# Kernel optimization log

Measured on AMD Instinct MI355X. Metric: run time of the kernel, lower is better.

Reference implementation:

```python
import jax, jax.numpy as jnp
import numpy as np

DIVERSITY_RATE = 0.5


def setup_inputs() -> dict:
    key = jax.random.key(0)
    k1, k2 = jax.random.split(key)
    # model log-probabilities at current step: (bsz, beam, vocab)
    lprobs = jax.nn.log_softmax(
        jax.random.normal(k1, (128, 5, 50257), dtype=jnp.float32), axis=-1
    )
    # historical hypothesis scores: (bsz, beam, step)
    scores = jax.random.normal(k2, (128, 5, 10), dtype=jnp.float32)
    return {"lprobs": lprobs, "scores": scores, "step": 10}


def reference(lprobs, scores, step):
    bsz, beam_size, vocab_size = lprobs.shape
    k = min(beam_size * 2, beam_size * vocab_size - 1)  # = 10 here

    # step > 0 path: accumulate running score of each hypothesis
    lp = lprobs + scores[:, :, step - 1][:, :, None]  # (bsz, beam, vocab)

    # 1/ per-beam top-k over vocab (vectorized over all beams at once)
    s, idx = jax.lax.top_k(lp, k)  # (bsz, beam, k); idx already < vocab (fmod no-op)

    # 2/,3/ intra-sibling ordering -> rank penalty (rank r gets r*rate)
    sibling_score = jnp.arange(1, k + 1, dtype=lp.dtype) * DIVERSITY_RATE  # (k,)
    s = s - sibling_score  # broadcast over (bsz, beam, k)

    # 4/ final top-k over all beam*k candidates
    indices = idx.reshape(bsz, beam_size * k)
    final_scores, flat_pos = jax.lax.top_k(s.reshape(bsz, beam_size * k), k)
    final_beams = flat_pos // k  # which input beam each winner came from
    final_indices = jnp.take_along_axis(indices, flat_pos, axis=1)  # vocab ids

    return final_scores, final_indices, final_beams
```

## Files before the change

### kernel.cpp

```cpp
#include <hip/hip_runtime.h>
#include <hip/hip_bf16.h>
#include <math.h>
#include <stdint.h>


#define BS   256
#define KK   10
#define BEAM 5
#define CAP  2048

typedef unsigned long long u64;

__device__ __forceinline__ uint32_t ford(float x) {
    uint32_t u = __float_as_uint(x);
    return (u & 0x80000000u) ? ~u : (u | 0x80000000u);
}
__device__ __forceinline__ float funord(uint32_t u) {
    return __uint_as_float((u & 0x80000000u) ? (u & 0x7fffffffu) : ~u);
}

__device__ __forceinline__ void merge_tree(u64* skey, int tid) {
    for (int off = BS / 2; off >= 1; off >>= 1) {
        if (tid < off) {
            const int pa = tid * KK, pb = (tid + off) * KK;
            u64 mk[KK];
            int ia = 0, ib = 0;
#pragma unroll
            for (int j = 0; j < KK; ++j) {
                u64 ka = skey[pa + ia], kb = skey[pb + ib];
                bool takeA = (ka >= kb);
                mk[j] = takeA ? ka : kb;
                if (takeA) ++ia; else ++ib;
            }
#pragma unroll
            for (int j = 0; j < KK; ++j) skey[pa + j] = mk[j];
        }
        __syncthreads();
    }
}

__global__ __launch_bounds__(BS) void dss_stage1(
    const float* __restrict__ lprobs,
    const float* __restrict__ scores,
    const int*   __restrict__ step_ptr,
    int vocab, int sdim,
    float* __restrict__ ws_val,
    int*   __restrict__ ws_idx)
{
    const int row = blockIdx.x;
    const int tid = threadIdx.x;
    const int step = step_ptr[0];
    const float bias = scores[(size_t)row * sdim + (step - 1)];
    const float* rp = lprobs + (size_t)row * vocab;

    __shared__ u64  cand[CAP];
    __shared__ u64  skey[BS * KK];
    __shared__ int  cnt;
    __shared__ float s_tau;

    int pre = (4 - (int)(((uintptr_t)rp >> 2) & 3)) & 3;
    if (pre > vocab) pre = vocab;
    const float4* p4 = (const float4*)(rp + pre);
    const int nvec = (vocab - pre) >> 2;
    const int done = pre + 4 * nvec;
    const int rem  = vocab - done;

    float m = -INFINITY;
    if (tid < pre) m = rp[tid];
#pragma unroll 4
    for (int t = tid; t < nvec; t += BS) {
        float4 x = p4[t];
        m = fmaxf(m, fmaxf(fmaxf(x.x, x.y), fmaxf(x.z, x.w)));
    }
    if (tid < rem) m = fmaxf(m, rp[done + tid]);

    {
        u64 key[KK];
        key[0] = ((u64)ford(m) << 32) | (uint32_t)~tid;
#pragma unroll
        for (int j = 1; j < KK; ++j) key[j] = 0;
#pragma unroll
        for (int j = 0; j < KK; ++j) skey[tid * KK + j] = key[j];
    }
    if (tid == 0) cnt = 0;
    __syncthreads();
    merge_tree(skey, tid);
    if (tid == 0) s_tau = funord((uint32_t)(skey[9] >> 32));
    __syncthreads();
    const float tau = s_tau;

    auto app = [&](float x, int i) {
        if (x >= tau) {
            int p = atomicAdd(&cnt, 1);
            if (p < CAP) cand[p] = ((u64)ford(x) << 32) | (uint32_t)~i;
        }
    };
    if (tid < pre) app(rp[tid], tid);
#pragma unroll 4
    for (int t = tid; t < nvec; t += BS) {
        float4 x = p4[t];
        int base = pre + 4 * t;
        if (x.x >= tau) app(x.x, base + 0);
        if (x.y >= tau) app(x.y, base + 1);
        if (x.z >= tau) app(x.z, base + 2);
        if (x.w >= tau) app(x.w, base + 3);
    }
    if (tid < rem) app(rp[done + tid], done + tid);
    __syncthreads();

    const int n = (cnt < CAP) ? cnt : CAP;
    {
        u64 key[KK];
#pragma unroll
        for (int j = 0; j < KK; ++j) key[j] = 0;
        for (int i = tid; i < n; i += BS) {
            u64 k = cand[i];
            if (k > key[KK - 1]) {
#pragma unroll
                for (int j = KK - 1; j >= 1; --j)
                    key[j] = (k > key[j - 1]) ? key[j - 1] : ((k > key[j]) ? k : key[j]);
                if (k > key[0]) key[0] = k;
            }
        }
#pragma unroll
        for (int j = 0; j < KK; ++j) skey[tid * KK + j] = key[j];
    }
    __syncthreads();
    merge_tree(skey, tid);

    if (tid < KK) {
        u64 k = skey[tid];
        ws_val[row * KK + tid] = funord((uint32_t)(k >> 32)) + bias;
        ws_idx[row * KK + tid] = (int)~(uint32_t)k;
    }
}

__global__ __launch_bounds__(64) void dss_stage2(
    const float* __restrict__ ws_val,
    const int*   __restrict__ ws_idx,
    float* __restrict__ out, int bsz)
{
    const int b = blockIdx.x;
    const int lane = threadIdx.x;

    float v = -INFINITY;
    int   vidx = 0;
    if (lane < BEAM * KK) {
        int beam = lane / KK;
        int r    = lane % KK;
        int o    = (b * BEAM + beam) * KK + r;
        v    = ws_val[o] - 0.5f * (float)(r + 1);
        vidx = ws_idx[o];
    }

    float* out_scores  = out;
    float* out_indices = out + (size_t)bsz * KK;
    float* out_beams   = out + 2 * (size_t)bsz * KK;

    for (int o = 0; o < KK; ++o) {
        float rv = v; int rp = lane;
#pragma unroll
        for (int off = 32; off >= 1; off >>= 1) {
            float ov = __shfl_xor(rv, off);
            int   op = __shfl_xor(rp, off);
            if (ov > rv || (ov == rv && op < rp)) { rv = ov; rp = op; }
        }
        int widx = __shfl(vidx, rp);
        if (lane == 0) {
            out_scores [b * KK + o] = rv;
            out_indices[b * KK + o] = (float)widx;
            out_beams  [b * KK + o] = (float)(rp / KK);
        }
        if (lane == rp) v = -INFINITY;
    }
}

extern "C" void kernel_launch(void* const* d_in, const int* in_sizes, int n_in,
                              void* d_out, int out_size, void* d_ws, size_t ws_size,
                              hipStream_t stream)
{
    const float* lprobs = (const float*)d_in[0];
    const float* scores = (const float*)d_in[1];
    const int*   step   = (const int*)d_in[2];

    const int bsz   = 128;
    const int rows  = bsz * BEAM;
    const int vocab = in_sizes[0] / rows;
    const int sdim  = in_sizes[1] / rows;

    float* ws_val = (float*)d_ws;
    int*   ws_idx = (int*)((char*)d_ws + (size_t)rows * KK * sizeof(float));

    dss_stage1<<<rows, BS, 0, stream>>>(lprobs, scores, step, vocab, sdim, ws_val, ws_idx);
    dss_stage2<<<bsz, 64, 0, stream>>>(ws_val, ws_idx, (float*)d_out, bsz);
}
```

Baseline: 225.8 us.

## Split each vocab row into chunks across blocks with LDS-staged two-pass top-k

Each row's vocab is split into up to 8 chunks, each handled by its own block, which gives 5120 blocks instead of 640 to fill the GPU. Every chunk block stages its slice in LDS so the second threshold pass reads shared memory rather than global memory. It picks the threshold with a wave-level shuffle top-10 in place of the tree merge. A new final kernel merges the per-chunk top-10 lists per beam and then runs the cross-beam selection. This trades extra workspace traffic and dynamic LDS use for more parallelism and a single global read of the input.

Measured after the change: 252.0 us. 1.12x slower.

```diff
diff --git a/kernel.cpp b/kernel.cpp
--- a/kernel.cpp
+++ b/kernel.cpp
@@ -7,7 +7,8 @@
 #define BS   256
 #define KK   10
 #define BEAM 5
-#define CAP  2048
+#define CAP  512
+#define FCAP 2048
 
 typedef unsigned long long u64;
 
@@ -19,33 +20,138 @@
     return __uint_as_float((u & 0x80000000u) ? (u & 0x7fffffffu) : ~u);
 }
 
-__device__ __forceinline__ void merge_tree(u64* skey, int tid) {
-    for (int off = BS / 2; off >= 1; off >>= 1) {
-        if (tid < off) {
-            const int pa = tid * KK, pb = (tid + off) * KK;
-            u64 mk[KK];
-            int ia = 0, ib = 0;
-#pragma unroll
-            for (int j = 0; j < KK; ++j) {
-                u64 ka = skey[pa + ia], kb = skey[pb + ib];
-                bool takeA = (ka >= kb);
-                mk[j] = takeA ? ka : kb;
-                if (takeA) ++ia; else ++ib;
-            }
-#pragma unroll
-            for (int j = 0; j < KK; ++j) skey[pa + j] = mk[j];
-        }
-        __syncthreads();
-    }
-}
-
-__global__ __launch_bounds__(BS) void dss_stage1(
+__device__ __forceinline__ void insert10(u64 (&key)[KK], u64 k) {
+    if (k > key[KK - 1]) {
+#pragma unroll
+        for (int j = KK - 1; j >= 1; --j)
+            key[j] = (k > key[j - 1]) ? key[j - 1] : ((k > key[j]) ? k : key[j]);
+        if (k > key[0]) key[0] = k;
+    }
+}
+
+extern __shared__ __align__(16) unsigned char smem_raw[];
+
+__global__ __launch_bounds__(BS) void dss_chunk_topk(
+    const float* __restrict__ lprobs,
+    const float* __restrict__ scores,
+    const int*   __restrict__ step_ptr,
+    int vocab, int sdim, int nc, int cs, int cap_f,
+    u64* __restrict__ ws_keys)
+{
+    const int chunk = blockIdx.x;
+    const int row   = blockIdx.y;
+    const int tid   = threadIdx.x;
+    const int lane  = tid & 63;
+    const int step  = step_ptr[0];
+    const float bias = scores[(size_t)row * sdim + (step - 1)];
+
+    const int c0 = chunk * cs;
+    int len = vocab - c0; if (len > cs) len = cs;
+    const float* rp = lprobs + (size_t)row * vocab + c0;
+
+    float* lds_f = (float*)smem_raw;
+    u64*   cand  = (u64*)(smem_raw + (size_t)cap_f * 4);
+    float* smax  = (float*)(cand + CAP);
+    int*   s_cnt = (int*)(smax + BS);
+    float* s_tau = (float*)(s_cnt + 1);
+
+    const int a0  = (int)(((uintptr_t)rp >> 2) & 3);
+    int pre = (4 - a0) & 3; if (pre > len) pre = len;
+    const float4* g4  = (const float4*)(rp + pre);
+    const int nvec = (len - pre) >> 2;
+    const int done = pre + 4 * nvec;
+    const int rem  = len - done;
+    float4* l4 = (float4*)(lds_f + a0 + pre);
+
+    float m = -INFINITY;
+    if (tid < pre) { float v = rp[tid] + bias; lds_f[a0 + tid] = v; m = v; }
+    for (int t = tid; t < nvec; t += BS) {
+        float4 x = g4[t];
+        x.x += bias; x.y += bias; x.z += bias; x.w += bias;
+        l4[t] = x;
+        m = fmaxf(m, fmaxf(fmaxf(x.x, x.y), fmaxf(x.z, x.w)));
+    }
+    if (tid < rem) { float v = rp[done + tid] + bias; lds_f[a0 + done + tid] = v; m = fmaxf(m, v); }
+
+    smax[tid] = m;
+    if (tid == 0) *s_cnt = 0;
+    __syncthreads();
+
+    if (tid < 64) {
+        float a = smax[lane], b = smax[lane + 64], c = smax[lane + 128], d = smax[lane + 192];
+        float t0;
+        if (a < b) { t0 = a; a = b; b = t0; }
+        if (c < d) { t0 = c; c = d; d = t0; }
+        if (a < c) { t0 = a; a = c; c = t0; }
+        if (b < d) { t0 = b; b = d; d = t0; }
+        if (b < c) { t0 = b; b = c; c = t0; }
+        float arr0 = a, arr1 = b, arr2 = c, arr3 = d;
+        float tau = -INFINITY;
+#pragma unroll
+        for (int r = 0; r < KK; ++r) {
+            float rv = arr0; int rl = lane;
+#pragma unroll
+            for (int o = 32; o >= 1; o >>= 1) {
+                float ov = __shfl_xor(rv, o);
+                int   ol = __shfl_xor(rl, o);
+                if (ov > rv || (ov == rv && ol < rl)) { rv = ov; rl = ol; }
+            }
+            if (lane == rl) { arr0 = arr1; arr1 = arr2; arr2 = arr3; arr3 = -INFINITY; }
+            tau = rv;
+        }
+        if (lane == 0) *s_tau = tau;
+    }
+    __syncthreads();
+    const float tau = *s_tau;
+
+    auto app = [&](float v, int j) {
+        int p = atomicAdd(s_cnt, 1);
+        if (p < CAP) cand[p] = ((u64)ford(v) << 32) | (uint32_t)~(c0 + j);
+    };
+    if (tid < pre) { float v = lds_f[a0 + tid]; if (v >= tau) app(v, tid); }
+    for (int t = tid; t < nvec; t += BS) {
+        float4 x = l4[t];
+        int base = pre + 4 * t;
+        if (x.x >= tau) app(x.x, base + 0);
+        if (x.y >= tau) app(x.y, base + 1);
+        if (x.z >= tau) app(x.z, base + 2);
+        if (x.w >= tau) app(x.w, base + 3);
+    }
+    if (tid < rem) { float v = lds_f[a0 + done + tid]; if (v >= tau) app(v, done + tid); }
+    __syncthreads();
+
+    if (tid < 64) {
+        int n = *s_cnt; if (n > CAP) n = CAP;
+        u64 key[KK];
+#pragma unroll
+        for (int j = 0; j < KK; ++j) key[j] = 0;
+        for (int i = lane; i < n; i += 64) insert10(key, cand[i]);
+        u64* outp = ws_keys + ((size_t)row * nc + chunk) * KK;
+#pragma unroll
+        for (int r = 0; r < KK; ++r) {
+            u64 rv = key[0]; int rl = lane;
+#pragma unroll
+            for (int o = 32; o >= 1; o >>= 1) {
+                u64 ov = __shfl_xor(rv, o);
+                int ol = __shfl_xor(rl, o);
+                if (ov > rv || (ov == rv && ol < rl)) { rv = ov; rl = ol; }
+            }
+            if (lane == rl) {
+#pragma unroll
+                for (int j = 0; j < KK - 1; ++j) key[j] = key[j + 1];
+                key[KK - 1] = 0;
+            }
+            if (lane == 0) outp[r] = rv;
+        }
+    }
+}
+
+__global__ __launch_bounds__(BS) void dss_row_topk(
     const float* __restrict__ lprobs,
     const float* __restrict__ scores,
     const int*   __restrict__ step_ptr,
     int vocab, int sdim,
-    float* __restrict__ ws_val,
-    int*   __restrict__ ws_idx)
+    u64* __restrict__ ws_keys)
 {
     const int row = blockIdx.x;
     const int tid = threadIdx.x;
@@ -53,10 +159,10 @@
     const float bias = scores[(size_t)row * sdim + (step - 1)];
     const float* rp = lprobs + (size_t)row * vocab;
 
-    __shared__ u64  cand[CAP];
+    __shared__ u64  cand[FCAP];
     __shared__ u64  skey[BS * KK];
     __shared__ int  cnt;
-    __shared__ float s_tau;
+    __shared__ float sh_tau;
 
     int pre = (4 - (int)(((uintptr_t)rp >> 2) & 3)) & 3;
     if (pre > vocab) pre = vocab;
@@ -66,112 +172,137 @@
     const int rem  = vocab - done;
 
     float m = -INFINITY;
-    if (tid < pre) m = rp[tid];
-#pragma unroll 4
+    if (tid < pre) m = rp[tid] + bias;
     for (int t = tid; t < nvec; t += BS) {
         float4 x = p4[t];
-        m = fmaxf(m, fmaxf(fmaxf(x.x, x.y), fmaxf(x.z, x.w)));
-    }
-    if (tid < rem) m = fmaxf(m, rp[done + tid]);
-
-    {
-        u64 key[KK];
-        key[0] = ((u64)ford(m) << 32) | (uint32_t)~tid;
-#pragma unroll
-        for (int j = 1; j < KK; ++j) key[j] = 0;
-#pragma unroll
-        for (int j = 0; j < KK; ++j) skey[tid * KK + j] = key[j];
-    }
+        m = fmaxf(m, fmaxf(fmaxf(x.x + bias, x.y + bias), fmaxf(x.z + bias, x.w + bias)));
+    }
+    if (tid < rem) m = fmaxf(m, rp[done + tid] + bias);
+
+    skey[tid * KK] = ((u64)ford(m) << 32) | (uint32_t)~tid;
+#pragma unroll
+    for (int j = 1; j < KK; ++j) skey[tid * KK + j] = 0;
     if (tid == 0) cnt = 0;
     __syncthreads();
-    merge_tree(skey, tid);
-    if (tid == 0) s_tau = funord((uint32_t)(skey[9] >> 32));
-    __syncthreads();
-    const float tau = s_tau;
-
-    auto app = [&](float x, int i) {
-        if (x >= tau) {
+    for (int off = BS / 2; off >= 1; off >>= 1) {
+        if (tid < off) {
+            const int pa = tid * KK, pb = (tid + off) * KK;
+            u64 mk[KK]; int ia = 0, ib = 0;
+#pragma unroll
+            for (int j = 0; j < KK; ++j) {
+                u64 ka = skey[pa + ia], kb = skey[pb + ib];
+                bool tA = (ka >= kb); mk[j] = tA ? ka : kb;
+                if (tA) ++ia; else ++ib;
+            }
+#pragma unroll
+            for (int j = 0; j < KK; ++j) skey[pa + j] = mk[j];
+        }
+        __syncthreads();
+    }
+    if (tid == 0) sh_tau = funord((uint32_t)(skey[9] >> 32));
+    __syncthreads();
+    const float tau = sh_tau;
+
+    auto app = [&](float v, int i) {
+        if (v >= tau) {
             int p = atomicAdd(&cnt, 1);
-            if (p < CAP) cand[p] = ((u64)ford(x) << 32) | (uint32_t)~i;
+            if (p < FCAP) cand[p] = ((u64)ford(v) << 32) | (uint32_t)~i;
         }
     };
-    if (tid < pre) app(rp[tid], tid);
-#pragma unroll 4
+    if (tid < pre) app(rp[tid] + bias, tid);
     for (int t = tid; t < nvec; t += BS) {
         float4 x = p4[t];
         int base = pre + 4 * t;
-        if (x.x >= tau) app(x.x, base + 0);
-        if (x.y >= tau) app(x.y, base + 1);
-        if (x.z >= tau) app(x.z, base + 2);
-        if (x.w >= tau) app(x.w, base + 3);
-    }
-    if (tid < rem) app(rp[done + tid], done + tid);
-    __syncthreads();
-
-    const int n = (cnt < CAP) ? cnt : CAP;
+        app(x.x + bias, base + 0); app(x.y + bias, base + 1);
+        app(x.z + bias, base + 2); app(x.w + bias, base + 3);
+    }
+    if (tid < rem) app(rp[done + tid] + bias, done + tid);
+    __syncthreads();
+
+    const int n = (cnt < FCAP) ? cnt : FCAP;
     {
         u64 key[KK];
 #pragma unroll
         for (int j = 0; j < KK; ++j) key[j] = 0;
-        for (int i = tid; i < n; i += BS) {
-            u64 k = cand[i];
-            if (k > key[KK - 1]) {
-#pragma unroll
-                for (int j = KK - 1; j >= 1; --j)
-                    key[j] = (k > key[j - 1]) ? key[j - 1] : ((k > key[j]) ? k : key[j]);
-                if (k > key[0]) key[0] = k;
-            }
-        }
+        for (int i = tid; i < n; i += BS) insert10(key, cand[i]);
 #pragma unroll
         for (int j = 0; j < KK; ++j) skey[tid * KK + j] = key[j];
     }
     __syncthreads();
-    merge_tree(skey, tid);
-
-    if (tid < KK) {
-        u64 k = skey[tid];
-        ws_val[row * KK + tid] = funord((uint32_t)(k >> 32)) + bias;
-        ws_idx[row * KK + tid] = (int)~(uint32_t)k;
-    }
-}
-
-__global__ __launch_bounds__(64) void dss_stage2(
-    const float* __restrict__ ws_val,
-    const int*   __restrict__ ws_idx,
-    float* __restrict__ out, int bsz)
+    for (int off = BS / 2; off >= 1; off >>= 1) {
+        if (tid < off) {
+            const int pa = tid * KK, pb = (tid + off) * KK;
+            u64 mk[KK]; int ia = 0, ib = 0;
+#pragma unroll
+            for (int j = 0; j < KK; ++j) {
+                u64 ka = skey[pa + ia], kb = skey[pb + ib];
+                bool tA = (ka >= kb); mk[j] = tA ? ka : kb;
+                if (tA) ++ia; else ++ib;
+            }
+#pragma unroll
+            for (int j = 0; j < KK; ++j) skey[pa + j] = mk[j];
+        }
+        __syncthreads();
+    }
+    if (tid < KK) ws_keys[(size_t)row * KK + tid] = skey[tid];
+}
+
+__global__ __launch_bounds__(BEAM * 64) void dss_final(
+    const u64* __restrict__ ws_keys,
+    float* __restrict__ out, int bsz, int nc)
 {
-    const int b = blockIdx.x;
-    const int lane = threadIdx.x;
-
-    float v = -INFINITY;
-    int   vidx = 0;
-    if (lane < BEAM * KK) {
-        int beam = lane / KK;
-        int r    = lane % KK;
-        int o    = (b * BEAM + beam) * KK + r;
-        v    = ws_val[o] - 0.5f * (float)(r + 1);
-        vidx = ws_idx[o];
-    }
-
-    float* out_scores  = out;
-    float* out_indices = out + (size_t)bsz * KK;
-    float* out_beams   = out + 2 * (size_t)bsz * KK;
-
-    for (int o = 0; o < KK; ++o) {
-        float rv = v; int rp = lane;
-#pragma unroll
-        for (int off = 32; off >= 1; off >>= 1) {
-            float ov = __shfl_xor(rv, off);
-            int   op = __shfl_xor(rp, off);
-            if (ov > rv || (ov == rv && op < rp)) { rv = ov; rp = op; }
-        }
-        int widx = __shfl(vidx, rp);
+    const int b    = blockIdx.x;
+    const int beam = threadIdx.x >> 6;
+    const int lane = threadIdx.x & 63;
+
+    __shared__ float s_pen[BEAM * KK];
+    __shared__ int   s_idx[BEAM * KK];
+
+    const int ncand = nc * KK;
+    const u64* kp = ws_keys + (size_t)(b * BEAM + beam) * ncand;
+    u64 c0 = (lane < ncand) ? kp[lane] : 0;
+    u64 c1 = (lane + 64 < ncand) ? kp[lane + 64] : 0;
+
+#pragma unroll
+    for (int r = 0; r < KK; ++r) {
+        u64 my = (c0 > c1) ? c0 : c1;
+        u64 rv = my; int rl = lane;
+#pragma unroll
+        for (int o = 32; o >= 1; o >>= 1) {
+            u64 ov = __shfl_xor(rv, o);
+            int ol = __shfl_xor(rl, o);
+            if (ov > rv || (ov == rv && ol < rl)) { rv = ov; rl = ol; }
+        }
+        if (lane == rl) { if (c0 == rv) c0 = 0; else c1 = 0; }
         if (lane == 0) {
-            out_scores [b * KK + o] = rv;
-            out_indices[b * KK + o] = (float)widx;
-            out_beams  [b * KK + o] = (float)(rp / KK);
-        }
-        if (lane == rp) v = -INFINITY;
+            s_pen[beam * KK + r] = funord((uint32_t)(rv >> 32)) - 0.5f * (float)(r + 1);
+            s_idx[beam * KK + r] = (int)~(uint32_t)rv;
+        }
+    }
+    __syncthreads();
+
+    if (threadIdx.x < 64) {
+        float v = -INFINITY; int vidx = 0;
+        if (lane < BEAM * KK) { v = s_pen[lane]; vidx = s_idx[lane]; }
+        float* out_scores  = out;
+        float* out_indices = out + (size_t)bsz * KK;
+        float* out_beams   = out + 2 * (size_t)bsz * KK;
+        for (int o = 0; o < KK; ++o) {
+            float rv = v; int rp = lane;
+#pragma unroll
+            for (int off = 32; off >= 1; off >>= 1) {
+                float ov = __shfl_xor(rv, off);
+                int   op = __shfl_xor(rp, off);
+                if (ov > rv || (ov == rv && op < rp)) { rv = ov; rp = op; }
+            }
+            int widx = __shfl(vidx, rp);
+            if (lane == 0) {
+                out_scores [b * KK + o] = rv;
+                out_indices[b * KK + o] = (float)widx;
+                out_beams  [b * KK + o] = (float)(rp / KK);
+            }
+            if (lane == rp) v = -INFINITY;
+        }
     }
 }
 
@@ -188,9 +319,20 @@
     const int vocab = in_sizes[0] / rows;
     const int sdim  = in_sizes[1] / rows;
 
-    float* ws_val = (float*)d_ws;
-    int*   ws_idx = (int*)((char*)d_ws + (size_t)rows * KK * sizeof(float));
-
-    dss_stage1<<<rows, BS, 0, stream>>>(lprobs, scores, step, vocab, sdim, ws_val, ws_idx);
-    dss_stage2<<<bsz, 64, 0, stream>>>(ws_val, ws_idx, (float*)d_out, bsz);
-}
+    u64* ws_keys = (u64*)d_ws;
+
+    int nc = 8;
+    if (ws_size < (size_t)rows * 8 * KK * sizeof(u64)) nc = 4;
+    if (ws_size < (size_t)rows * 4 * KK * sizeof(u64)) nc = 1;
+
+    if (nc > 1) {
+        const int cs = (vocab + nc - 1) / nc;
+        const int cap_f = (cs + 3 + 3) & ~3;
+        const size_t smem = (size_t)cap_f * 4 + (size_t)CAP * 8 + BS * 4 + 16;
+        dss_chunk_topk<<<dim3(nc, rows), BS, smem, stream>>>(
+            lprobs, scores, step, vocab, sdim, nc, cs, cap_f, ws_keys);
+    } else {
+        dss_row_topk<<<rows, BS, 0, stream>>>(lprobs, scores, step, vocab, sdim, ws_keys);
+    }
+    dss_final<<<bsz, BEAM * 64, 0, stream>>>(ws_keys, (float*)d_out, bsz, nc);
+}
```
